# Performance work log

Measured on AMD Instinct MI355X. Metric: run time of the kernel, lower is better.

The kernel has to match this reference:

```python
import jax, jax.numpy as jnp
import numpy as np

B, S, D, E, K = 4, 2048, 1024, 8, 2
H = 4 * D  # expert hidden dim


def setup_inputs() -> dict:
    key = jax.random.key(0)
    ks = jax.random.split(key, 4)
    sc = lambda n: 1.0 / np.sqrt(n)
    return {
        "x": jax.random.normal(ks[0], (B, S, D), jnp.float32),
        "gate_w": jax.random.normal(ks[1], (D, E), jnp.float32) * sc(D),
        "gate_b": jnp.zeros((E,), jnp.float32),
        "w1": jax.random.normal(ks[2], (E, D, H), jnp.float32) * sc(D),
        "b1": jnp.zeros((E, H), jnp.float32),
        "w2": jax.random.normal(ks[3], (E, H, D), jnp.float32) * sc(H),
        "b2": jnp.zeros((E, D), jnp.float32),
    }


def reference(x, gate_w, gate_b, w1, b1, w2, b2):
    Bx, Sx, Dx = x.shape
    n_exp = w1.shape[0]

    # --- TopKRouter: softmax over expert logits, keep top-k scores at their slots ---
    logits = jnp.einsum('bsd,de->bse', x, gate_w) + gate_b          # [B,S,E]
    scores = jax.nn.softmax(logits, axis=-1)
    topk_s, topk_i = jax.lax.top_k(scores, K)                        # [B,S,K]
    onehot = jax.nn.one_hot(topk_i, n_exp, dtype=scores.dtype)       # [B,S,K,E]
    dispatch = jnp.einsum('bske,bsk->bse', onehot, topk_s)           # [B,S,E]

    # --- DynamicMoE combine ---
    xf = x.reshape(-1, Dx)                                           # [B*S, D]
    wf = dispatch.reshape(-1, n_exp)                                 # [B*S, E]
    out = jnp.zeros_like(xf)
    for i in range(n_exp):  # fixed small expert count; sequential overwrite semantics
        wi = wf[:, i:i + 1]                                          # [B*S, 1]
        # routing weight multiplies the expert INPUT (as in the original)
        h = jax.nn.relu((xf * wi) @ w1[i] + b1[i])                   # [B*S, 4D]
        y = h @ w2[i] + b2[i]                                        # [B*S, D]
        # out[mask] = y : later experts overwrite earlier ones
        out = jnp.where(wi > 0, y, out)
    return out.reshape(Bx, Sx, Dx)
```

## Files before the change

kernel.cpp:

```cpp
#include <hip/hip_runtime.h>
#include <hip/hip_bf16.h>
#include <stdint.h>

typedef __attribute__((ext_vector_type(8))) __bf16 bf16x8;
typedef __attribute__((ext_vector_type(4))) __bf16 bf16x4;
typedef __attribute__((ext_vector_type(4))) float  f32x4;

#define NTOK   8192
#define DMODEL 1024
#define HDIM   4096
#define NEXP   8

__device__ __forceinline__ void glds16(const void* g, void* l) {
  __builtin_amdgcn_global_load_lds(
      (const __attribute__((address_space(1))) uint32_t*)g,
      (__attribute__((address_space(3))) uint32_t*)l, 16, 0, 0);
}

#define WAITV(N) asm volatile("s_waitcnt vmcnt(" #N ")" ::: "memory")
#define SBAR()  do { __builtin_amdgcn_sched_barrier(0); \
                     __builtin_amdgcn_s_barrier();      \
                     __builtin_amdgcn_sched_barrier(0); } while (0)

__global__ void zero_cnt_kernel(int* cnt) {
  if (threadIdx.x < NEXP) cnt[threadIdx.x] = 0;
}

__global__ void prefix_kernel(const int* __restrict__ cnt, int* __restrict__ base) {
  if (threadIdx.x == 0) {
    int b = 0;
    base[0] = 0;
    for (int e = 0; e < NEXP; ++e) {
      b += (cnt[e] + 127) & ~127;
      base[e + 1] = b;
    }
  }
}

__global__ __launch_bounds__(256) void moe_gate_kernel(
    const float* __restrict__ x, const float* __restrict__ gw,
    const float* __restrict__ gb, float* __restrict__ wgt,
    int* __restrict__ cnt, int* __restrict__ meta)
{
  const int lane = threadIdx.x & 63;
  const int wv   = threadIdx.x >> 6;
  const int t    = (blockIdx.x << 2) + wv;
  const float* xp = x + (size_t)t * DMODEL;

  float acc[NEXP];
#pragma unroll
  for (int e = 0; e < NEXP; ++e) acc[e] = 0.f;

#pragma unroll
  for (int j = 0; j < DMODEL / 64; ++j) {
    const int d = (j << 6) + lane;
    const float xv = xp[d];
    const float4 g0 = *(const float4*)(gw + (size_t)d * NEXP);
    const float4 g1 = *(const float4*)(gw + (size_t)d * NEXP + 4);
    acc[0] = fmaf(xv, g0.x, acc[0]);
    acc[1] = fmaf(xv, g0.y, acc[1]);
    acc[2] = fmaf(xv, g0.z, acc[2]);
    acc[3] = fmaf(xv, g0.w, acc[3]);
    acc[4] = fmaf(xv, g1.x, acc[4]);
    acc[5] = fmaf(xv, g1.y, acc[5]);
    acc[6] = fmaf(xv, g1.z, acc[6]);
    acc[7] = fmaf(xv, g1.w, acc[7]);
  }
#pragma unroll
  for (int e = 0; e < NEXP; ++e) {
#pragma unroll
    for (int off = 32; off > 0; off >>= 1)
      acc[e] += __shfl_xor(acc[e], off, 64);
  }
  if (lane == 0) {
    float l[NEXP];
#pragma unroll
    for (int e = 0; e < NEXP; ++e) l[e] = acc[e] + gb[e];
    int i1 = 0; float m1 = l[0];
#pragma unroll
    for (int e = 1; e < NEXP; ++e) if (l[e] > m1) { m1 = l[e]; i1 = e; }
    int i2 = -1; float m2 = -3.402823466e38f;
#pragma unroll
    for (int e = 0; e < NEXP; ++e) if (e != i1 && l[e] > m2) { m2 = l[e]; i2 = e; }
    const int es = i1 > i2 ? i1 : i2;
    float s = 0.f;
#pragma unroll
    for (int e = 0; e < NEXP; ++e) s += expf(l[e] - m1);
    const float w = expf(l[es] - m1) / s;
    wgt[t] = w;
    const int pos = atomicAdd(&cnt[es], 1);
    meta[t] = (es << 13) | pos;
  }
}

__global__ __launch_bounds__(256) void pack_x_kernel(
    const float* __restrict__ x, const float* __restrict__ wgt,
    const int* __restrict__ meta, const int* __restrict__ base,
    __bf16* __restrict__ xbf, int* __restrict__ sortmap)
{
  const int t = blockIdx.x * 2 + (threadIdx.x >> 7);
  const int l = threadIdx.x & 127;
  const int m = meta[t];
  const int es = m >> 13, pos = m & 8191;
  const int dst = base[es] + pos;
  const float w = wgt[t];
  const float4 a = *(const float4*)(x + (size_t)t * DMODEL + l * 8);
  const float4 b = *(const float4*)(x + (size_t)t * DMODEL + l * 8 + 4);
  bf16x8 o;
  o[0] = (__bf16)(a.x * w); o[1] = (__bf16)(a.y * w);
  o[2] = (__bf16)(a.z * w); o[3] = (__bf16)(a.w * w);
  o[4] = (__bf16)(b.x * w); o[5] = (__bf16)(b.y * w);
  o[6] = (__bf16)(b.z * w); o[7] = (__bf16)(b.w * w);
  *(bf16x8*)(xbf + (size_t)dst * DMODEL + l * 8) = o;
  if (l == 0) sortmap[dst] = t;
}

__global__ __launch_bounds__(256) void zeropad_kernel(
    const int* __restrict__ cnt, const int* __restrict__ base,
    __bf16* __restrict__ xbf)
{
  const int e = blockIdx.x;
  const int c0 = cnt[e], cp = base[e + 1] - base[e];
  bf16x4 z; z[0] = z[1] = z[2] = z[3] = (__bf16)0.f;
  for (int r = c0; r < cp; ++r)
    *(bf16x4*)(xbf + (size_t)(base[e] + r) * DMODEL + threadIdx.x * 4) = z;
}

template<int N, int K>
__global__ __launch_bounds__(256) void pack_w_kernel(
    const float* __restrict__ src, __bf16* __restrict__ dst)
{
  const int k0 = blockIdx.x * 64, np = blockIdx.y, e = blockIdx.z;
  const int t = threadIdx.x;
  __shared__ __bf16 sh[8192];

  const float* sp = src + (size_t)e * K * N + (size_t)k0 * N + np * 128;
#pragma unroll
  for (int i = 0; i < 8; ++i) {
    const int id = i * 256 + t;
    const int k = id >> 5, n4 = id & 31;
    const float4 v = *(const float4*)(sp + (size_t)k * N + n4 * 4);
    const int phys = n4 ^ ((k & 3) << 3);
    bf16x4 o; o[0] = (__bf16)v.x; o[1] = (__bf16)v.y;
              o[2] = (__bf16)v.z; o[3] = (__bf16)v.w;
    *(bf16x4*)&sh[k * 128 + phys * 4] = o;
  }
  __syncthreads();

  __bf16* dbase = dst + ((size_t)(e * (N / 128) + np) * 128) * K + k0;
#pragma unroll
  for (int j2 = 0; j2 < 4; ++j2) {
    const int c = j2 * 256 + t;
    const int n = c >> 3, ks8 = c & 7;
    bf16x8 v;
#pragma unroll
    for (int j = 0; j < 8; ++j) {
      const int k = ks8 * 8 + j;
      v[j] = sh[k * 128 + (((n >> 2) ^ ((k & 3) << 3)) << 2) + (n & 3)];
    }
    *(bf16x8*)(dbase + (size_t)n * K + ks8 * 8) = v;
  }
}

template<int KSTEPS, int ASTRIDE, int NOUT, bool RELU, bool SCATTER, typename OutT>
__global__ __launch_bounds__(256, 2) void moe_gemm_kernel(
    const __bf16* __restrict__ Am, const __bf16* __restrict__ Bp,
    const float* __restrict__ bias, const int* __restrict__ cnt,
    const int* __restrict__ base, const int* __restrict__ sortmap,
    OutT* __restrict__ outp)
{
  const int e  = blockIdx.z;
  const int ce = cnt[e];
  const int rb = base[e];
  const int cep = base[e + 1] - rb;
  const int m0 = blockIdx.y << 7;
  if (m0 >= cep) return;
  const int np = blockIdx.x, n0 = np << 7;

  const int tid = threadIdx.x, lane = tid & 63, wv = tid >> 6;
  const int wm = wv >> 1, wn = wv & 1;

  __shared__ alignas(16) __bf16 lds[32768];

  const __bf16* asrc[4];
  const __bf16* bsrc[4];
#pragma unroll
  for (int i = 0; i < 4; ++i) {
    const int c = (wv * 4 + i) * 64 + lane;
    const int r = c >> 3, p = c & 7;
    const int koff = (p ^ (r & 7)) * 8;
    asrc[i] = Am + (size_t)(rb + m0 + r) * ASTRIDE + koff;
    bsrc[i] = Bp + ((size_t)(e * (NOUT / 128) + np) * 128 + r) * ASTRIDE + koff;
  }

  auto stage = [&](int buf, int ks) {
    __bf16* Ad = lds + buf * 16384;
    __bf16* Bd = Ad + 8192;
#pragma unroll
    for (int i = 0; i < 4; ++i)
      glds16(asrc[i] + ks * 64, Ad + (wv * 4 + i) * 512);
#pragma unroll
    for (int i = 0; i < 4; ++i)
      glds16(bsrc[i] + ks * 64, Bd + (wv * 4 + i) * 512);
  };

  const int cl = lane & 15, rh = (lane >> 4) << 2;
  float bb[4];
#pragma unroll
  for (int j = 0; j < 4; ++j)
    bb[j] = bias[(size_t)e * NOUT + n0 + wn * 64 + j * 16 + cl];

  f32x4 acc[4][4] = {};
  const int rl = lane & 15, sl = lane >> 4;

  auto compute = [&](int buf) {
    const char* Ab = (const char*)(lds + buf * 16384);
    const char* Bb = Ab + 16384;
#pragma unroll
    for (int kk = 0; kk < 2; ++kk) {
      bf16x8 af[4], bfv[4];
#pragma unroll
      for (int f = 0; f < 4; ++f) {
        const int r = wm * 64 + f * 16 + rl;
        af[f] = *(const bf16x8*)(Ab + r * 128 + (((kk * 4 + sl) ^ (r & 7)) << 4));
      }
#pragma unroll
      for (int f = 0; f < 4; ++f) {
        const int r = wn * 64 + f * 16 + rl;
        bfv[f] = *(const bf16x8*)(Bb + r * 128 + (((kk * 4 + sl) ^ (r & 7)) << 4));
      }
#pragma unroll
      for (int i = 0; i < 4; ++i)
#pragma unroll
        for (int j = 0; j < 4; ++j)
          acc[i][j] = __builtin_amdgcn_mfma_f32_16x16x32_bf16(af[i], bfv[j], acc[i][j], 0, 0, 0);
    }
  };

  stage(0, 0);
  int cur = 0;
  for (int ks = 0; ks < KSTEPS; ++ks) {
    if (ks + 1 < KSTEPS) {
      stage(cur ^ 1, ks + 1);
      WAITV(8);
    } else {
      WAITV(0);
    }
    SBAR();
    compute(cur);
    __builtin_amdgcn_sched_barrier(0);
    __builtin_amdgcn_s_barrier();
    cur ^= 1;
  }

#pragma unroll
  for (int i = 0; i < 4; ++i) {
#pragma unroll
    for (int r = 0; r < 4; ++r) {
      const int gm = m0 + wm * 64 + i * 16 + rh + r;
      if constexpr (SCATTER) {
        if (gm < ce) {
          const int tok = sortmap[rb + gm];
          OutT* op = outp + (size_t)tok * NOUT + n0 + wn * 64;
#pragma unroll
          for (int j = 0; j < 4; ++j)
            op[j * 16 + cl] = (OutT)(acc[i][j][r] + bb[j]);
        }
      } else {
        OutT* op = outp + (size_t)(rb + gm) * NOUT + n0 + wn * 64;
        const bool live = gm < ce;
#pragma unroll
        for (int j = 0; j < 4; ++j) {
          float v = acc[i][j][r] + bb[j];
          if constexpr (RELU) v = fmaxf(v, 0.f);
          op[j * 16 + cl] = live ? (OutT)v : (OutT)0.f;
        }
      }
    }
  }
}

extern "C" void kernel_launch(void* const* d_in, const int* in_sizes, int n_in,
                              void* d_out, int out_size, void* d_ws, size_t ws_size,
                              hipStream_t stream)
{
  const float* x  = (const float*)d_in[0];
  const float* gw = (const float*)d_in[1];
  const float* gb = (const float*)d_in[2];
  const float* w1 = (const float*)d_in[3];
  const float* b1 = (const float*)d_in[4];
  const float* w2 = (const float*)d_in[5];
  const float* b2 = (const float*)d_in[6];
  float* out = (float*)d_out;

  char* ws = (char*)d_ws;
  int*    cnt     = (int*)ws;
  int*    base    = (int*)(ws + 256);
  int*    meta    = (int*)(ws + 4096);
  float*  wgt     = (float*)(ws + 40960);
  int*    sortmap = (int*)(ws + 81920);
  __bf16* xbf     = (__bf16*)(ws + ((size_t)1  << 20));
  __bf16* hmat    = (__bf16*)(ws + ((size_t)20 << 20));
  __bf16* wp      = (__bf16*)(ws + ((size_t)92 << 20));

  zero_cnt_kernel<<<1, 64, 0, stream>>>(cnt);
  moe_gate_kernel<<<NTOK / 4, 256, 0, stream>>>(x, gw, gb, wgt, cnt, meta);
  prefix_kernel<<<1, 64, 0, stream>>>(cnt, base);
  pack_x_kernel<<<NTOK / 2, 256, 0, stream>>>(x, wgt, meta, base, xbf, sortmap);
  zeropad_kernel<<<NEXP, 256, 0, stream>>>(cnt, base, xbf);

  pack_w_kernel<HDIM, DMODEL><<<dim3(DMODEL / 64, HDIM / 128, NEXP), 256, 0, stream>>>(w1, wp);
  moe_gemm_kernel<DMODEL / 64, DMODEL, HDIM, true, false, __bf16>
      <<<dim3(HDIM / 128, NTOK / 128, NEXP), 256, 0, stream>>>(
          xbf, wp, b1, cnt, base, sortmap, hmat);

  pack_w_kernel<DMODEL, HDIM><<<dim3(HDIM / 64, DMODEL / 128, NEXP), 256, 0, stream>>>(w2, wp);
  moe_gemm_kernel<HDIM / 64, HDIM, DMODEL, false, true, float>
      <<<dim3(DMODEL / 128, NTOK / 128, NEXP), 256, 0, stream>>>(
          hmat, wp, b2, cnt, base, sortmap, out);
}
```

Baseline: 408.5 us.

## Enlarge MoE GEMM tiles to 256x256 with 512-thread blocks

Replaces the 128x128, 4-wave expert GEMM with a 256x256 tile computed by 8 waves. Each wave now holds an 8x4 fragment accumulator, which raises data reuse per LDS and global load. Per-expert padding grows to 256 rows, and the workspace offsets and grid sizes change to match. The double-buffered loop now uses one barrier per k-step and raises wave priority around the MFMA bursts. In exchange it uses 128KB of LDS and runs one block per CU, and it wastes more work on padded rows.

```diff
diff --git a/kernel.cpp b/kernel.cpp
--- a/kernel.cpp
+++ b/kernel.cpp
@@ -31,7 +31,7 @@
     int b = 0;
     base[0] = 0;
     for (int e = 0; e < NEXP; ++e) {
-      b += (cnt[e] + 127) & ~127;
+      b += (cnt[e] + 255) & ~255;
       base[e + 1] = b;
     }
   }
@@ -163,7 +163,7 @@
 }
 
 template<int KSTEPS, int ASTRIDE, int NOUT, bool RELU, bool SCATTER, typename OutT>
-__global__ __launch_bounds__(256, 2) void moe_gemm_kernel(
+__global__ __launch_bounds__(512, 1) void moe_gemm256_kernel(
     const __bf16* __restrict__ Am, const __bf16* __restrict__ Bp,
     const float* __restrict__ bias, const int* __restrict__ cnt,
     const int* __restrict__ base, const int* __restrict__ sortmap,
@@ -173,14 +173,15 @@
   const int ce = cnt[e];
   const int rb = base[e];
   const int cep = base[e + 1] - rb;
-  const int m0 = blockIdx.y << 7;
+  const int m0 = blockIdx.y << 8;
   if (m0 >= cep) return;
-  const int np = blockIdx.x, n0 = np << 7;
+  const int np = blockIdx.x, n0 = np << 8;
 
   const int tid = threadIdx.x, lane = tid & 63, wv = tid >> 6;
-  const int wm = wv >> 1, wn = wv & 1;
-
-  __shared__ alignas(16) __bf16 lds[32768];
+  const int wm = wv >> 2, wn = wv & 3;
+  const int rl = lane & 15, sl = lane >> 4;
+
+  __shared__ alignas(16) __bf16 lds[65536];
 
   const __bf16* asrc[4];
   const __bf16* bsrc[4];
@@ -190,12 +191,12 @@
     const int r = c >> 3, p = c & 7;
     const int koff = (p ^ (r & 7)) * 8;
     asrc[i] = Am + (size_t)(rb + m0 + r) * ASTRIDE + koff;
-    bsrc[i] = Bp + ((size_t)(e * (NOUT / 128) + np) * 128 + r) * ASTRIDE + koff;
+    bsrc[i] = Bp + ((size_t)(e * (NOUT / 128) + np * 2) * 128 + r) * ASTRIDE + koff;
   }
 
   auto stage = [&](int buf, int ks) {
-    __bf16* Ad = lds + buf * 16384;
-    __bf16* Bd = Ad + 8192;
+    __bf16* Ad = lds + buf * 32768;
+    __bf16* Bd = Ad + 16384;
 #pragma unroll
     for (int i = 0; i < 4; ++i)
       glds16(asrc[i] + ks * 64, Ad + (wv * 4 + i) * 512);
@@ -204,76 +205,73 @@
       glds16(bsrc[i] + ks * 64, Bd + (wv * 4 + i) * 512);
   };
 
-  const int cl = lane & 15, rh = (lane >> 4) << 2;
+  f32x4 acc[8][4] = {};
+
+  stage(0, 0);
+  for (int ks = 0; ks < KSTEPS; ++ks) {
+    const int buf = ks & 1;
+    WAITV(0);
+    SBAR();
+    if (ks + 1 < KSTEPS) stage(buf ^ 1, ks + 1);
+
+    const char* Ab = (const char*)lds + buf * 65536 + wm * 16384;
+    const char* Bb = (const char*)lds + buf * 65536 + 32768 + (wn >> 1) * 16384;
+
+#pragma unroll
+    for (int kk = 0; kk < 2; ++kk) {
+      bf16x8 af[8];
+#pragma unroll
+      for (int mf = 0; mf < 8; ++mf) {
+        const int row = mf * 16 + rl;
+        af[mf] = *(const bf16x8*)(Ab + row * 128 + (((kk * 4 + sl) ^ (row & 7)) << 4));
+      }
+#pragma unroll
+      for (int nh = 0; nh < 2; ++nh) {
+        bf16x8 bf[2];
+#pragma unroll
+        for (int nf2 = 0; nf2 < 2; ++nf2) {
+          const int row = (wn & 1) * 64 + nh * 32 + nf2 * 16 + rl;
+          bf[nf2] = *(const bf16x8*)(Bb + row * 128 + (((kk * 4 + sl) ^ (row & 7)) << 4));
+        }
+        __builtin_amdgcn_s_setprio(1);
+#pragma unroll
+        for (int mf = 0; mf < 8; ++mf)
+#pragma unroll
+          for (int nf2 = 0; nf2 < 2; ++nf2)
+            acc[mf][nh * 2 + nf2] = __builtin_amdgcn_mfma_f32_16x16x32_bf16(
+                af[mf], bf[nf2], acc[mf][nh * 2 + nf2], 0, 0, 0);
+        __builtin_amdgcn_s_setprio(0);
+      }
+    }
+  }
+
+  const int cl = rl;
   float bb[4];
 #pragma unroll
-  for (int j = 0; j < 4; ++j)
-    bb[j] = bias[(size_t)e * NOUT + n0 + wn * 64 + j * 16 + cl];
-
-  f32x4 acc[4][4] = {};
-  const int rl = lane & 15, sl = lane >> 4;
-
-  auto compute = [&](int buf) {
-    const char* Ab = (const char*)(lds + buf * 16384);
-    const char* Bb = Ab + 16384;
-#pragma unroll
-    for (int kk = 0; kk < 2; ++kk) {
-      bf16x8 af[4], bfv[4];
-#pragma unroll
-      for (int f = 0; f < 4; ++f) {
-        const int r = wm * 64 + f * 16 + rl;
-        af[f] = *(const bf16x8*)(Ab + r * 128 + (((kk * 4 + sl) ^ (r & 7)) << 4));
-      }
-#pragma unroll
-      for (int f = 0; f < 4; ++f) {
-        const int r = wn * 64 + f * 16 + rl;
-        bfv[f] = *(const bf16x8*)(Bb + r * 128 + (((kk * 4 + sl) ^ (r & 7)) << 4));
-      }
-#pragma unroll
-      for (int i = 0; i < 4; ++i)
-#pragma unroll
-        for (int j = 0; j < 4; ++j)
-          acc[i][j] = __builtin_amdgcn_mfma_f32_16x16x32_bf16(af[i], bfv[j], acc[i][j], 0, 0, 0);
-    }
-  };
-
-  stage(0, 0);
-  int cur = 0;
-  for (int ks = 0; ks < KSTEPS; ++ks) {
-    if (ks + 1 < KSTEPS) {
-      stage(cur ^ 1, ks + 1);
-      WAITV(8);
-    } else {
-      WAITV(0);
-    }
-    SBAR();
-    compute(cur);
-    __builtin_amdgcn_sched_barrier(0);
-    __builtin_amdgcn_s_barrier();
-    cur ^= 1;
-  }
-
-#pragma unroll
-  for (int i = 0; i < 4; ++i) {
-#pragma unroll
-    for (int r = 0; r < 4; ++r) {
-      const int gm = m0 + wm * 64 + i * 16 + rh + r;
+  for (int nf = 0; nf < 4; ++nf)
+    bb[nf] = bias[(size_t)e * NOUT + n0 + wn * 64 + nf * 16 + cl];
+
+#pragma unroll
+  for (int mf = 0; mf < 8; ++mf) {
+#pragma unroll
+    for (int j = 0; j < 4; ++j) {
+      const int gm = m0 + wm * 128 + mf * 16 + sl * 4 + j;
       if constexpr (SCATTER) {
         if (gm < ce) {
           const int tok = sortmap[rb + gm];
           OutT* op = outp + (size_t)tok * NOUT + n0 + wn * 64;
 #pragma unroll
-          for (int j = 0; j < 4; ++j)
-            op[j * 16 + cl] = (OutT)(acc[i][j][r] + bb[j]);
+          for (int nf = 0; nf < 4; ++nf)
+            op[nf * 16 + cl] = (OutT)(acc[mf][nf][j] + bb[nf]);
         }
       } else {
         OutT* op = outp + (size_t)(rb + gm) * NOUT + n0 + wn * 64;
         const bool live = gm < ce;
 #pragma unroll
-        for (int j = 0; j < 4; ++j) {
-          float v = acc[i][j][r] + bb[j];
+        for (int nf = 0; nf < 4; ++nf) {
+          float v = acc[mf][nf][j] + bb[nf];
           if constexpr (RELU) v = fmaxf(v, 0.f);
-          op[j * 16 + cl] = live ? (OutT)v : (OutT)0.f;
+          op[nf * 16 + cl] = live ? (OutT)v : (OutT)0.f;
         }
       }
     }
@@ -299,9 +297,9 @@
   int*    meta    = (int*)(ws + 4096);
   float*  wgt     = (float*)(ws + 40960);
   int*    sortmap = (int*)(ws + 81920);
-  __bf16* xbf     = (__bf16*)(ws + ((size_t)1  << 20));
-  __bf16* hmat    = (__bf16*)(ws + ((size_t)20 << 20));
-  __bf16* wp      = (__bf16*)(ws + ((size_t)92 << 20));
+  __bf16* xbf     = (__bf16*)(ws + ((size_t)1   << 20));
+  __bf16* hmat    = (__bf16*)(ws + ((size_t)22  << 20));
+  __bf16* wp      = (__bf16*)(ws + ((size_t)104 << 20));
 
   zero_cnt_kernel<<<1, 64, 0, stream>>>(cnt);
   moe_gate_kernel<<<NTOK / 4, 256, 0, stream>>>(x, gw, gb, wgt, cnt, meta);
@@ -310,12 +308,12 @@
   zeropad_kernel<<<NEXP, 256, 0, stream>>>(cnt, base, xbf);
 
   pack_w_kernel<HDIM, DMODEL><<<dim3(DMODEL / 64, HDIM / 128, NEXP), 256, 0, stream>>>(w1, wp);
-  moe_gemm_kernel<DMODEL / 64, DMODEL, HDIM, true, false, __bf16>
-      <<<dim3(HDIM / 128, NTOK / 128, NEXP), 256, 0, stream>>>(
+  moe_gemm256_kernel<DMODEL / 64, DMODEL, HDIM, true, false, __bf16>
+      <<<dim3(HDIM / 256, 40, NEXP), 512, 0, stream>>>(
           xbf, wp, b1, cnt, base, sortmap, hmat);
 
   pack_w_kernel<DMODEL, HDIM><<<dim3(HDIM / 64, DMODEL / 128, NEXP), 256, 0, stream>>>(w2, wp);
-  moe_gemm_kernel<HDIM / 64, HDIM, DMODEL, false, true, float>
-      <<<dim3(DMODEL / 128, NTOK / 128, NEXP), 256, 0, stream>>>(
+  moe_gemm256_kernel<HDIM / 64, HDIM, DMODEL, false, true, float>
+      <<<dim3(DMODEL / 256, 40, NEXP), 512, 0, stream>>>(
           hmat, wp, b2, cnt, base, sortmap, out);
 }
```

New measurement: 417.8 us. 2.3% more time.
